# Optimization experiments

Hardware: AMD Instinct MI355X
Metric: run time of the kernel (lower is better)

The kernel has to match this reference:

```python
import jax, jax.numpy as jnp
import numpy as np

BN_EPS = 1e-5

def _square_distance(a, b):
    # a: (B,N,3), b: (B,M,3) -> (B,N,M) squared euclidean distance
    a2 = jnp.sum(a * a, axis=-1)[:, :, None]
    b2 = jnp.sum(b * b, axis=-1)[:, None, :]
    return a2 + b2 - 2.0 * jnp.einsum('bnd,bmd->bnm', a, b)

def _bn(x, gamma, beta, mean, var):
    # eval-mode batchnorm over channel (last) dim
    return (x - mean) * jax.lax.rsqrt(var + BN_EPS) * gamma + beta

def setup_inputs() -> dict:
    key = jax.random.key(0)
    ks = jax.random.split(key, 16)
    B, M, N, D, C = 4, 2048, 16384, 64, 64
    din, dout = C + D, 64
    return {
        'xyz_down': jax.random.normal(ks[0], (B, M, 3), jnp.float32),
        'xyz_up': jax.random.normal(ks[1], (B, N, 3), jnp.float32),
        'feat_down': jax.random.normal(ks[2], (B, M, D), jnp.float32),
        'feat_up': jax.random.normal(ks[3], (B, N, C), jnp.float32),
        'W1': jax.random.normal(ks[4], (din, din), jnp.float32) * 0.05,
        'b1': jax.random.normal(ks[5], (din,), jnp.float32) * 0.05,
        'bn1_gamma': jax.random.uniform(ks[6], (din,), jnp.float32, 0.5, 1.5),
        'bn1_beta': jax.random.normal(ks[7], (din,), jnp.float32) * 0.05,
        'bn1_mean': jax.random.normal(ks[8], (din,), jnp.float32) * 0.05,
        'bn1_var': jax.random.uniform(ks[9], (din,), jnp.float32, 0.5, 1.5),
        'W2': jax.random.normal(ks[10], (dout, din), jnp.float32) * 0.05,
        'b2': jax.random.normal(ks[11], (dout,), jnp.float32) * 0.05,
        'bn2_gamma': jax.random.uniform(ks[12], (dout,), jnp.float32, 0.5, 1.5),
        'bn2_beta': jax.random.normal(ks[13], (dout,), jnp.float32) * 0.05,
        'bn2_mean': jax.random.normal(ks[14], (dout,), jnp.float32) * 0.05,
        'bn2_var': jax.random.uniform(ks[15], (dout,), jnp.float32, 0.5, 1.5),
    }

def reference(xyz_down, xyz_up, feat_down, feat_up,
              W1, b1, bn1_gamma, bn1_beta, bn1_mean, bn1_var,
              W2, b2, bn2_gamma, bn2_beta, bn2_mean, bn2_var):
    dist = _square_distance(xyz_up, xyz_down)              # (B,N,M)
    dist_recip = 1.0 / (dist + 1e-8)
    weight = dist_recip / jnp.sum(dist_recip, axis=2, keepdims=True)
    # bmm-equivalent of the original broadcast-multiply-sum
    feat_interp = jnp.einsum('bnm,bmd->bnd', weight, feat_down)  # (B,N,D)
    x = jnp.concatenate([feat_up, feat_interp], axis=-1)   # (B,N,C+D)
    # Conv1d(k=1) == pointwise linear over channel dim
    x = jnp.einsum('bnc,oc->bno', x, W1) + b1
    x = jax.nn.relu(_bn(x, bn1_gamma, bn1_beta, bn1_mean, bn1_var))
    x = jnp.einsum('bnc,oc->bno', x, W2) + b2
    x = _bn(x, bn2_gamma, bn2_beta, bn2_mean, bn2_var)
    return x
```

## Files before the change

kernel.cpp:

```cpp
#include <hip/hip_runtime.h>

typedef unsigned short u16;
typedef unsigned int   u32;
typedef unsigned long long u64;

typedef __attribute__((ext_vector_type(8))) short bf16x8;
typedef __attribute__((ext_vector_type(4))) float f32x4;
typedef __attribute__((ext_vector_type(2))) float f32x2;

#define BB 4
#define MM 2048
#define NN 16384
#define DD 64

__device__ __forceinline__ u16 f2bf(float f) {
    union { float f; u32 u; } v; v.f = f;
    u32 r = v.u + 0x7fffu + ((v.u >> 16) & 1u);
    return (u16)(r >> 16);
}

__device__ __forceinline__ u32 pack_trunc(float hi, float lo) {
    union { float f; u32 u; } a, b; a.f = hi; b.f = lo;
    return __builtin_amdgcn_perm(a.u, b.u, 0x07060302);
}

__device__ __forceinline__ u32 pack_rne(float hi, float lo) {
    return (u32)f2bf(lo) | ((u32)f2bf(hi) << 16);
}

__device__ __forceinline__ bf16x8 pack8(float4 p, float4 q) {
    bf16x8 v;
    v[0] = (short)f2bf(p.x); v[1] = (short)f2bf(p.y);
    v[2] = (short)f2bf(p.z); v[3] = (short)f2bf(p.w);
    v[4] = (short)f2bf(q.x); v[5] = (short)f2bf(q.y);
    v[6] = (short)f2bf(q.z); v[7] = (short)f2bf(q.w);
    return v;
}

#define OFF_FDT   0ull
#define OFF_XYZP  1048576ull
#define OFF_W1S   1179648ull
#define OFF_W2S   1212416ull
#define OFF_BN    1228800ull
#define WS_NEED   1230336ull

__global__ __launch_bounds__(256)
void prep6_kernel(const float* __restrict__ xyz_down,
                  const float* __restrict__ feat_down,
                  const float* __restrict__ W1, const float* __restrict__ b1,
                  const float* __restrict__ g1, const float* __restrict__ be1,
                  const float* __restrict__ m1, const float* __restrict__ v1,
                  const float* __restrict__ W2, const float* __restrict__ b2,
                  const float* __restrict__ g2, const float* __restrict__ be2,
                  const float* __restrict__ m2, const float* __restrict__ v2,
                  u16* __restrict__ fdT, float4* __restrict__ xyzP,
                  u16* __restrict__ w1s, u16* __restrict__ w2s,
                  float* __restrict__ bnbuf)
{
    const int blk = blockIdx.x, t = threadIdx.x;
    if (blk < 256) {
        __shared__ u16 T[32 * 72];
        const int b = blk >> 6, m0 = (blk & 63) * 32;
        {
            const int row = t >> 3, seg = (t & 7) * 8;
            const float4* src = (const float4*)(feat_down + ((size_t)(b * MM + m0 + row)) * 64 + seg);
            float4 v0 = src[0], v1 = src[1];
            bf16x8 pk = pack8(v0, v1);
            *(bf16x8*)&T[row * 72 + seg] = pk;
        }
        __syncthreads();
        {
            const int d = t & 63, w = t >> 6;
            union { u16 h[8]; uint4 q; } o;
#pragma unroll
            for (int j = 0; j < 8; j++) o.h[j] = T[(w * 8 + j) * 72 + d];
            *(uint4*)&fdT[((size_t)(b * 64 + d)) * MM + m0 + w * 8] = o.q;
        }
    } else if (blk < 272) {
        int g = (blk - 256) * 256 + t;
        int b = g >> 10, p = g & 1023;
        const float* s = xyz_down + ((size_t)b * MM + 2 * p) * 3;
        float x0 = s[0], y0 = s[1], z0 = s[2];
        float x1 = s[3], y1 = s[4], z1 = s[5];
        float w0 = x0 * x0 + y0 * y0 + z0 * z0 + 1e-8f;
        float w1v = x1 * x1 + y1 * y1 + z1 * z1 + 1e-8f;
        xyzP[(size_t)g * 2 + 0] = make_float4(-2.f * x0, -2.f * x1, -2.f * y0, -2.f * y1);
        xyzP[(size_t)g * 2 + 1] = make_float4(-2.f * z0, -2.f * z1, w0, w1v);
    } else if (blk < 280) {
        int slot = (blk - 272) * 256 + t;
        int f = slot >> 6, l = slot & 63;
        int kg = f >> 3, ot = f & 7;
        int o = ot * 16 + (l & 15), c = kg * 32 + (l >> 4) * 8;
        const float4* src = (const float4*)(W1 + (size_t)o * 128 + c);
        bf16x8 v = pack8(src[0], src[1]);
        *(bf16x8*)&w1s[(size_t)slot * 8] = v;
    } else if (blk < 284) {
        int slot = (blk - 280) * 256 + t;
        int f = slot >> 6, l = slot & 63;
        int kg = f >> 2, ot = f & 3;
        int o = ot * 16 + (l & 15), c = kg * 32 + (l >> 4) * 8;
        const float4* src = (const float4*)(W2 + (size_t)o * 128 + c);
        bf16x8 v = pack8(src[0], src[1]);
        *(bf16x8*)&w2s[(size_t)slot * 8] = v;
    } else {
        if (t < 128) {
            float a = g1[t] * rsqrtf(v1[t] + 1e-5f);
            bnbuf[t] = a;
            bnbuf[128 + t] = (b1[t] - m1[t]) * a + be1[t];
        } else if (t < 192) {
            int o = t - 128;
            float a = g2[o] * rsqrtf(v2[o] + 1e-5f);
            bnbuf[256 + o] = a;
            bnbuf[320 + o] = (b2[o] - m2[o]) * a + be2[o];
        }
    }
}

__global__ __launch_bounds__(256, 2)
void fused7_kernel(const float* __restrict__ xyz_up,
                   const u16* __restrict__ fdT,
                   const float4* __restrict__ xyzP,
                   const float* __restrict__ feat_up,
                   const u16* __restrict__ w1s,
                   const u16* __restrict__ w2s,
                   const float* __restrict__ bnbuf,
                   float* __restrict__ out)
{
    __shared__ u16   ftbuf[2][64 * 72];
    __shared__ float xyzb[2][32 * 12];
    __shared__ u16   xh[128 * 136];
    __shared__ float bnl[384];

    const int tid = threadIdx.x;
    const int b  = blockIdx.x >> 7;
    const int n0 = (blockIdx.x & 127) * 128;
    const int wave = tid >> 6;
    const int lane = tid & 63;
    const int q    = lane >> 4;
    const int nl   = lane & 15;

    bnl[tid] = bnbuf[tid];
    if (tid < 128) bnl[256 + tid] = bnbuf[256 + tid];

    {
        const int r = tid >> 1, sg = (tid & 1) * 32;
        const float4* fs = (const float4*)(feat_up + ((size_t)(b * NN + n0 + r)) * 64 + sg);
        float4 f0 = fs[0], f1 = fs[1], f2 = fs[2], f3 = fs[3];
        float4 f4 = fs[4], f5 = fs[5], f6 = fs[6], f7 = fs[7];
        uint4 o0, o1;
        o0.x = pack_rne(f0.y, f0.x); o0.y = pack_rne(f0.w, f0.z);
        o0.z = pack_rne(f1.y, f1.x); o0.w = pack_rne(f1.w, f1.z);
        o1.x = pack_rne(f2.y, f2.x); o1.y = pack_rne(f2.w, f2.z);
        o1.z = pack_rne(f3.y, f3.x); o1.w = pack_rne(f3.w, f3.z);
        uint4* xd = (uint4*)&xh[r * 136 + sg];
        xd[0] = o0; xd[1] = o1;
        uint4 o2, o3;
        o2.x = pack_rne(f4.y, f4.x); o2.y = pack_rne(f4.w, f4.z);
        o2.z = pack_rne(f5.y, f5.x); o2.w = pack_rne(f5.w, f5.z);
        o3.x = pack_rne(f6.y, f6.x); o3.y = pack_rne(f6.w, f6.z);
        o3.z = pack_rne(f7.y, f7.x); o3.w = pack_rne(f7.w, f7.z);
        xd[2] = o2; xd[3] = o3;
    }

    float ax[2], ay[2], az[2];
    f32x2 a22[2];
#pragma unroll
    for (int rt = 0; rt < 2; rt++) {
        const int row = n0 + wave * 32 + rt * 16 + nl;
        const float* xu = xyz_up + ((size_t)(b * NN + row)) * 3;
        ax[rt] = xu[0]; ay[rt] = xu[1]; az[rt] = xu[2];
        float a2 = ax[rt] * ax[rt] + ay[rt] * ay[rt] + az[rt] * az[rt];
        a22[rt] = (f32x2){a2, a2};
    }
    const f32x2 eps2 = (f32x2){1e-8f, 1e-8f};

    f32x4 acc[2][4];
#pragma unroll
    for (int rt = 0; rt < 2; rt++)
#pragma unroll
        for (int i = 0; i < 4; i++) acc[rt][i] = (f32x4){0.f, 0.f, 0.f, 0.f};
    f32x4 accd[2];
    accd[0] = (f32x4){0.f, 0.f, 0.f, 0.f};
    accd[1] = (f32x4){0.f, 0.f, 0.f, 0.f};

    bf16x8 ones;
#pragma unroll
    for (int i = 0; i < 8; i++) ones[i] = (short)0x3F80;

    const int sd = tid >> 2, sms = (tid & 3) * 16;
    const u16* fsrc = fdT + ((size_t)(b * 64 + sd)) * MM + sms;
    const float4* xsrc = xyzP + ((size_t)b * 1024 + (tid >> 1)) * 2 + (tid & 1);
    float* xdst = &xyzb[0][0] + (tid >> 1) * 12 + (tid & 1) * 4;

    {
        u16* fd = &ftbuf[0][sd * 72 + sms];
        *(uint4*)fd       = *(const uint4*)(fsrc);
        *(uint4*)(fd + 8) = *(const uint4*)(fsrc + 8);
        if (tid < 64) *(float4*)xdst = xsrc[0];
    }
    __syncthreads();

    for (int c = 0; c < 32; ++c) {
        const int cur = c & 1, nxt = cur ^ 1;
        const bool have_next = (c + 1) < 32;
        uint4 nf0, nf1; float4 nx;
        if (have_next) {
            const int mc = (c + 1) * 64;
            nf0 = *(const uint4*)(fsrc + mc);
            nf1 = *(const uint4*)(fsrc + mc + 8);
            if (tid < 64) nx = xsrc[(size_t)(c + 1) * 64];
        }

#pragma unroll
        for (int kk = 0; kk < 2; kk++) {
            u32 fr[2][4];
#pragma unroll
            for (int jp = 0; jp < 4; jp++) {
                const int pi = kk * 16 + q * 4 + jp;
                const float* base = &xyzb[cur][pi * 12];
                float4 ld0 = *(const float4*)(base);
                float4 ld1 = *(const float4*)(base + 4);
                f32x2 px = (f32x2){ld0.x, ld0.y};
                f32x2 py = (f32x2){ld0.z, ld0.w};
                f32x2 pz = (f32x2){ld1.x, ld1.y};
                f32x2 pw = (f32x2){ld1.z, ld1.w};
#pragma unroll
                for (int rt = 0; rt < 2; rt++) {
                    f32x2 d = __builtin_elementwise_fma(px, (f32x2){ax[rt], ax[rt]},
                              __builtin_elementwise_fma(py, (f32x2){ay[rt], ay[rt]},
                              __builtin_elementwise_fma(pz, (f32x2){az[rt], az[rt]},
                                                        pw + a22[rt])));
                    d = __builtin_elementwise_max(d, eps2);
                    float r0 = __builtin_amdgcn_rcpf(d.x);
                    float r1 = __builtin_amdgcn_rcpf(d.y);
                    fr[rt][jp] = pack_trunc(r1, r0);
                }
            }
            bf16x8 bb[4];
#pragma unroll
            for (int dt = 0; dt < 4; dt++)
                bb[dt] = *(bf16x8*)&ftbuf[cur][(dt * 16 + nl) * 72 + kk * 32 + q * 8];
#pragma unroll
            for (int rt = 0; rt < 2; rt++) {
                union { u32 u[4]; bf16x8 v; } af;
                af.u[0] = fr[rt][0]; af.u[1] = fr[rt][1];
                af.u[2] = fr[rt][2]; af.u[3] = fr[rt][3];
#pragma unroll
                for (int dt = 0; dt < 4; dt++)
                    acc[rt][dt] = __builtin_amdgcn_mfma_f32_16x16x32_bf16(af.v, bb[dt], acc[rt][dt], 0, 0, 0);
                accd[rt] = __builtin_amdgcn_mfma_f32_16x16x32_bf16(af.v, ones, accd[rt], 0, 0, 0);
            }
        }

        if (have_next) {
            u16* fd = &ftbuf[nxt][sd * 72 + sms];
            *(uint4*)fd       = nf0;
            *(uint4*)(fd + 8) = nf1;
            if (tid < 64) *(float4*)(&xyzb[nxt][0] + (tid >> 1) * 12 + (tid & 1) * 4) = nx;
        }
        __syncthreads();
    }

#pragma unroll
    for (int rt = 0; rt < 2; rt++)
#pragma unroll
    for (int reg = 0; reg < 4; reg++) {
        float inv = 1.0f / accd[rt][reg];
        int rl = wave * 32 + rt * 16 + q * 4 + reg;
#pragma unroll
        for (int dt = 0; dt < 4; dt++)
            xh[rl * 136 + 64 + dt * 16 + nl] = f2bf(acc[rt][dt][reg] * inv);
    }

    f32x4 acc1[2][8];
#pragma unroll
    for (int rt = 0; rt < 2; rt++)
#pragma unroll
        for (int i = 0; i < 8; i++) acc1[rt][i] = (f32x4){0.f, 0.f, 0.f, 0.f};
#pragma unroll
    for (int kg = 0; kg < 4; kg++) {
        bf16x8 afr[2];
#pragma unroll
        for (int rt = 0; rt < 2; rt++)
            afr[rt] = *(bf16x8*)&xh[(wave * 32 + rt * 16 + nl) * 136 + kg * 32 + q * 8];
#pragma unroll
        for (int ot = 0; ot < 8; ot++) {
            bf16x8 bf = *(const bf16x8*)(w1s + ((size_t)(kg * 8 + ot) * 64 + lane) * 8);
            acc1[0][ot] = __builtin_amdgcn_mfma_f32_16x16x32_bf16(afr[0], bf, acc1[0][ot], 0, 0, 0);
            acc1[1][ot] = __builtin_amdgcn_mfma_f32_16x16x32_bf16(afr[1], bf, acc1[1][ot], 0, 0, 0);
        }
    }
#pragma unroll
    for (int ot = 0; ot < 8; ot++) {
        int o = ot * 16 + nl;
        float aa = bnl[o], bc = bnl[128 + o];
#pragma unroll
        for (int rt = 0; rt < 2; rt++)
#pragma unroll
        for (int reg = 0; reg < 4; reg++) {
            float v = fmaxf(fmaf(acc1[rt][ot][reg], aa, bc), 0.f);
            xh[(wave * 32 + rt * 16 + q * 4 + reg) * 136 + o] = f2bf(v);
        }
    }

    f32x4 acc2[2][4];
#pragma unroll
    for (int rt = 0; rt < 2; rt++)
#pragma unroll
        for (int i = 0; i < 4; i++) acc2[rt][i] = (f32x4){0.f, 0.f, 0.f, 0.f};
#pragma unroll
    for (int kg = 0; kg < 4; kg++) {
        bf16x8 afr[2];
#pragma unroll
        for (int rt = 0; rt < 2; rt++)
            afr[rt] = *(bf16x8*)&xh[(wave * 32 + rt * 16 + nl) * 136 + kg * 32 + q * 8];
#pragma unroll
        for (int ot = 0; ot < 4; ot++) {
            bf16x8 bf = *(const bf16x8*)(w2s + ((size_t)(kg * 4 + ot) * 64 + lane) * 8);
            acc2[0][ot] = __builtin_amdgcn_mfma_f32_16x16x32_bf16(afr[0], bf, acc2[0][ot], 0, 0, 0);
            acc2[1][ot] = __builtin_amdgcn_mfma_f32_16x16x32_bf16(afr[1], bf, acc2[1][ot], 0, 0, 0);
        }
    }
    float* of = (float*)xh;
#pragma unroll
    for (int ot = 0; ot < 4; ot++) {
        int o = ot * 16 + nl;
        float aa = bnl[256 + o], bc = bnl[320 + o];
#pragma unroll
        for (int rt = 0; rt < 2; rt++)
#pragma unroll
        for (int reg = 0; reg < 4; reg++)
            of[(wave * 32 + rt * 16 + q * 4 + reg) * 68 + o] = fmaf(acc2[rt][ot][reg], aa, bc);
    }

    {
        const int r = tid >> 1, sg = (tid & 1) * 32;
        const float4* sf = (const float4*)&of[r * 68 + sg];
        float4* dst = (float4*)(out + ((size_t)(b * NN + n0 + r)) * 64 + sg);
#pragma unroll
        for (int i = 0; i < 8; i++) dst[i] = sf[i];
    }
}

#define TN 128
#define BM 64
#define RS 72
#define FS 72

__global__ __launch_bounds__(256, 3)
void interp_kernel(const float* __restrict__ xyz_down,
                   const float* __restrict__ xyz_up,
                   const float* __restrict__ feat_down,
                   u16* __restrict__ interp_out)
{
    __shared__ u16   rbuf[TN * RS];
    __shared__ u16   ftbuf[DD * FS];
    __shared__ float xyzb[BM * 3];
    __shared__ float denp[TN * 2];
    __shared__ float invden[TN];

    const int tid = threadIdx.x;
    const int b  = blockIdx.x >> 7;
    const int n0 = (blockIdx.x & 127) * TN;

    const int nl_r = tid >> 1;
    const int half = tid & 1;
    const float* xu = xyz_up + (size_t)(b * NN + n0 + nl_r) * 3;
    const float ax = xu[0], ay = xu[1], az = xu[2];

    denp[tid] = 0.f;

    const int wave = tid >> 6;
    const int lane = tid & 63;
    const int q    = lane >> 4;
    const int nl   = lane & 15;

    f32x4 acc[2][4];
#pragma unroll
    for (int i = 0; i < 2; i++)
#pragma unroll
        for (int j = 0; j < 4; j++) acc[i][j] = (f32x4){0.f, 0.f, 0.f, 0.f};

    const int sm = (tid & 31) * 2;
    const int sd = (tid >> 5) * 8;

    for (int mc = 0; mc < MM; mc += BM) {
        __syncthreads();
        if (tid < 192) xyzb[tid] = xyz_down[(size_t)(b * MM + mc) * 3 + tid];
        {
            const float4* f0 = (const float4*)(feat_down + (size_t)(b * MM + mc + sm) * DD + sd);
            const float4* f1 = (const float4*)(feat_down + (size_t)(b * MM + mc + sm + 1) * DD + sd);
            float4 a0 = f0[0], a1 = f0[1];
            float4 b0 = f1[0], b1 = f1[1];
            float r0[8] = {a0.x, a0.y, a0.z, a0.w, a1.x, a1.y, a1.z, a1.w};
            float r1[8] = {b0.x, b0.y, b0.z, b0.w, b1.x, b1.y, b1.z, b1.w};
#pragma unroll
            for (int j = 0; j < 8; j++) {
                u32 pk = (u32)f2bf(r0[j]) | ((u32)f2bf(r1[j]) << 16);
                *(u32*)&ftbuf[(sd + j) * FS + sm] = pk;
            }
        }
        __syncthreads();
        {
            float dlc = 0.f;
#pragma unroll
            for (int s = 0; s < 4; s++) {
                bf16x8 v;
#pragma unroll
                for (int j = 0; j < 8; j++) {
                    int m = half * 32 + s * 8 + j;
                    float dx = ax - xyzb[3 * m + 0];
                    float dy = ay - xyzb[3 * m + 1];
                    float dz = az - xyzb[3 * m + 2];
                    float d = fmaf(dx, dx, fmaf(dy, dy, dz * dz)) + 1e-8f;
                    float r = __builtin_amdgcn_rcpf(d);
                    dlc += r;
                    v[j] = (short)f2bf(r);
                }
                *(bf16x8*)&rbuf[nl_r * RS + half * 32 + s * 8] = v;
            }
            denp[nl_r * 2 + half] += dlc;
        }
        __syncthreads();
        {
            const int rowbase = wave * 32;
#pragma unroll
            for (int k0 = 0; k0 < BM; k0 += 32) {
                bf16x8 a0 = *(bf16x8*)&rbuf[(rowbase + nl) * RS + k0 + q * 8];
                bf16x8 a1 = *(bf16x8*)&rbuf[(rowbase + 16 + nl) * RS + k0 + q * 8];
#pragma unroll
                for (int dt = 0; dt < 4; dt++) {
                    bf16x8 bb = *(bf16x8*)&ftbuf[(dt * 16 + nl) * FS + k0 + q * 8];
                    acc[0][dt] = __builtin_amdgcn_mfma_f32_16x16x32_bf16(a0, bb, acc[0][dt], 0, 0, 0);
                    acc[1][dt] = __builtin_amdgcn_mfma_f32_16x16x32_bf16(a1, bb, acc[1][dt], 0, 0, 0);
                }
            }
        }
    }

    __syncthreads();
    if (tid < TN) invden[tid] = 1.0f / (denp[tid * 2] + denp[tid * 2 + 1]);
    __syncthreads();
    {
        const int rowbase = wave * 32;
#pragma unroll
        for (int nt = 0; nt < 2; nt++) {
#pragma unroll
            for (int reg = 0; reg < 4; reg++) {
                int nloc = rowbase + nt * 16 + q * 4 + reg;
                float inv = invden[nloc];
                size_t gbase = (size_t)(b * NN + n0 + nloc) * DD;
#pragma unroll
                for (int dt = 0; dt < 4; dt++)
                    interp_out[gbase + dt * 16 + nl] = f2bf(acc[nt][dt][reg] * inv);
            }
        }
    }
}

#define T2 64

__global__ __launch_bounds__(256, 1)
void mlp_kernel(const float* __restrict__ feat_up,
                const u16*   __restrict__ interp,
                const float* __restrict__ W1, const float* __restrict__ b1,
                const float* __restrict__ g1, const float* __restrict__ be1,
                const float* __restrict__ m1, const float* __restrict__ v1,
                const float* __restrict__ W2, const float* __restrict__ b2,
                const float* __restrict__ g2, const float* __restrict__ be2,
                const float* __restrict__ m2, const float* __restrict__ v2,
                float* __restrict__ out)
{
    __shared__ u16 xb[T2 * 136];
    __shared__ u16 hb[T2 * 136];
    __shared__ u16 w1b[128 * 136];
    __shared__ u16 w2b[64 * 136];
    __shared__ float A1[128], Bc1[128], A2[64], Bc2[64];

    const int tid = threadIdx.x;
    const int b  = blockIdx.x >> 8;
    const int n0 = (blockIdx.x & 255) * T2;
    const int wave = tid >> 6;
    const int lane = tid & 63;
    const int q    = lane >> 4;
    const int nl   = lane & 15;

    if (tid < 128) {
        float a = g1[tid] * rsqrtf(v1[tid] + 1e-5f);
        A1[tid]  = a;
        Bc1[tid] = (b1[tid] - m1[tid]) * a + be1[tid];
    } else if (tid < 192) {
        int o = tid - 128;
        float a = g2[o] * rsqrtf(v2[o] + 1e-5f);
        A2[o]  = a;
        Bc2[o] = (b2[o] - m2[o]) * a + be2[o];
    }
    {
        const float4* src = (const float4*)(W1 + (size_t)(tid >> 1) * 128 + (tid & 1) * 64);
        u16* dst = &w1b[(tid >> 1) * 136 + (tid & 1) * 64];
#pragma unroll
        for (int i = 0; i < 8; i++)
            *(bf16x8*)(dst + 8 * i) = pack8(src[2 * i], src[2 * i + 1]);
    }
    {
        const float4* src = (const float4*)(W2 + (size_t)(tid >> 2) * 128 + (tid & 3) * 32);
        u16* dst = &w2b[(tid >> 2) * 136 + (tid & 3) * 32];
#pragma unroll
        for (int i = 0; i < 4; i++)
            *(bf16x8*)(dst + 8 * i) = pack8(src[2 * i], src[2 * i + 1]);
    }
    if (tid < 128) {
        int n = tid >> 1, hf = tid & 1;
        const float4* src = (const float4*)(feat_up + (size_t)(b * NN + n0 + n) * 64 + hf * 32);
        u16* dst = &xb[n * 136 + hf * 32];
#pragma unroll
        for (int i = 0; i < 4; i++)
            *(bf16x8*)(dst + 8 * i) = pack8(src[2 * i], src[2 * i + 1]);
    } else {
        int t2 = tid - 128;
        int n = t2 >> 1, hf = t2 & 1;
        const uint4* src = (const uint4*)(interp + (size_t)(b * NN + n0 + n) * 64 + hf * 32);
        u16* dst = &xb[n * 136 + 64 + hf * 32];
#pragma unroll
        for (int i = 0; i < 4; i++)
            *(uint4*)(dst + 8 * i) = src[i];
    }
    __syncthreads();

    f32x4 acc1[8];
#pragma unroll
    for (int i = 0; i < 8; i++) acc1[i] = (f32x4){0.f, 0.f, 0.f, 0.f};
#pragma unroll
    for (int k0 = 0; k0 < 128; k0 += 32) {
        bf16x8 a = *(bf16x8*)&xb[(wave * 16 + nl) * 136 + k0 + q * 8];
#pragma unroll
        for (int ot = 0; ot < 8; ot++) {
            bf16x8 bb = *(bf16x8*)&w1b[(ot * 16 + nl) * 136 + k0 + q * 8];
            acc1[ot] = __builtin_amdgcn_mfma_f32_16x16x32_bf16(a, bb, acc1[ot], 0, 0, 0);
        }
    }
#pragma unroll
    for (int ot = 0; ot < 8; ot++) {
        int o = ot * 16 + nl;
        float aa = A1[o], bc = Bc1[o];
#pragma unroll
        for (int reg = 0; reg < 4; reg++) {
            float v = fmaxf(fmaf(acc1[ot][reg], aa, bc), 0.f);
            hb[(wave * 16 + q * 4 + reg) * 136 + o] = f2bf(v);
        }
    }
    __syncthreads();

    f32x4 acc2[4];
#pragma unroll
    for (int i = 0; i < 4; i++) acc2[i] = (f32x4){0.f, 0.f, 0.f, 0.f};
#pragma unroll
    for (int k0 = 0; k0 < 128; k0 += 32) {
        bf16x8 a = *(bf16x8*)&hb[(wave * 16 + nl) * 136 + k0 + q * 8];
#pragma unroll
        for (int ot = 0; ot < 4; ot++) {
            bf16x8 bb = *(bf16x8*)&w2b[(ot * 16 + nl) * 136 + k0 + q * 8];
            acc2[ot] = __builtin_amdgcn_mfma_f32_16x16x32_bf16(a, bb, acc2[ot], 0, 0, 0);
        }
    }
#pragma unroll
    for (int ot = 0; ot < 4; ot++) {
        int o = ot * 16 + nl;
        float aa = A2[o], bc = Bc2[o];
#pragma unroll
        for (int reg = 0; reg < 4; reg++)
            out[(size_t)(b * NN + n0 + wave * 16 + q * 4 + reg) * 64 + o] =
                fmaf(acc2[ot][reg], aa, bc);
    }
}

extern "C" void kernel_launch(void* const* d_in, const int* in_sizes, int n_in,
                              void* d_out, int out_size, void* d_ws, size_t ws_size,
                              hipStream_t stream) {
    const float* xyz_down  = (const float*)d_in[0];
    const float* xyz_up    = (const float*)d_in[1];
    const float* feat_down = (const float*)d_in[2];
    const float* feat_up   = (const float*)d_in[3];
    const float* W1  = (const float*)d_in[4];
    const float* b1  = (const float*)d_in[5];
    const float* g1  = (const float*)d_in[6];
    const float* be1 = (const float*)d_in[7];
    const float* m1  = (const float*)d_in[8];
    const float* v1  = (const float*)d_in[9];
    const float* W2  = (const float*)d_in[10];
    const float* b2  = (const float*)d_in[11];
    const float* g2  = (const float*)d_in[12];
    const float* be2 = (const float*)d_in[13];
    const float* m2  = (const float*)d_in[14];
    const float* v2  = (const float*)d_in[15];
    float* out = (float*)d_out;
    char* ws = (char*)d_ws;

    if (ws_size >= WS_NEED) {
        u16*    fdT   = (u16*)(ws + OFF_FDT);
        float4* xyzP  = (float4*)(ws + OFF_XYZP);
        u16*    w1s   = (u16*)(ws + OFF_W1S);
        u16*    w2s   = (u16*)(ws + OFF_W2S);
        float*  bnbuf = (float*)(ws + OFF_BN);

        prep6_kernel<<<dim3(285), dim3(256), 0, stream>>>(
            xyz_down, feat_down, W1, b1, g1, be1, m1, v1,
            W2, b2, g2, be2, m2, v2, fdT, xyzP, w1s, w2s, bnbuf);
        fused7_kernel<<<dim3(BB * (NN / 128)), dim3(256), 0, stream>>>(
            xyz_up, fdT, xyzP, feat_up, w1s, w2s, bnbuf, out);
    } else {
        u16* interp = (u16*)d_ws;
        interp_kernel<<<dim3(BB * (NN / TN)), dim3(256), 0, stream>>>(
            xyz_down, xyz_up, feat_down, interp);
        mlp_kernel<<<dim3(BB * (NN / T2)), dim3(256), 0, stream>>>(
            feat_up, interp, W1, b1, g1, be1, m1, v1,
            W2, b2, g2, be2, m2, v2, out);
    }
}
```

Baseline: 148.8 us.

## Split interpolation K-dimension across two wave halves with 512-thread blocks

Doubles the block to 512 threads. The two halves of the waves each process half of every 64-point chunk of the M reduction, and their partial accumulators and denominators are combined through shared memory before normalization. Shared buffers are aliased into one smem region to cut LDS use, the feat_up load is deferred until after the main loop, and the MLP stage is split so each wave handles 16 rows. The aim is higher occupancy and more parallelism per tile, at the cost of an extra LDS reduction and more barriers.

```diff
diff --git a/kernel.cpp b/kernel.cpp
--- a/kernel.cpp
+++ b/kernel.cpp
@@ -116,8 +116,8 @@
     }
 }
 
-__global__ __launch_bounds__(256, 2)
-void fused7_kernel(const float* __restrict__ xyz_up,
+__global__ __launch_bounds__(512, 4)
+void fused8_kernel(const float* __restrict__ xyz_up,
                    const u16* __restrict__ fdT,
                    const float4* __restrict__ xyzP,
                    const float* __restrict__ feat_up,
@@ -126,168 +126,179 @@
                    const float* __restrict__ bnbuf,
                    float* __restrict__ out)
 {
-    __shared__ u16   ftbuf[2][64 * 72];
-    __shared__ float xyzb[2][32 * 12];
-    __shared__ u16   xh[128 * 136];
+    __shared__ __align__(16) char smem[34816];
     __shared__ float bnl[384];
-
-    const int tid = threadIdx.x;
-    const int b  = blockIdx.x >> 7;
-    const int n0 = (blockIdx.x & 127) * 128;
+    u16*   const ftbuf = (u16*)smem;
+    float* const xyzb  = (float*)(smem + 18432);
+    u16*   const xh    = (u16*)smem;
+    float* const of    = (float*)smem;
+
+    const int tid  = threadIdx.x;
+    const int b    = blockIdx.x >> 7;
+    const int n0   = (blockIdx.x & 127) * 128;
     const int wave = tid >> 6;
     const int lane = tid & 63;
     const int q    = lane >> 4;
     const int nl   = lane & 15;
-
-    bnl[tid] = bnbuf[tid];
-    if (tid < 128) bnl[256 + tid] = bnbuf[256 + tid];
+    const int rg   = wave & 3;
+    const int h    = wave >> 2;
+
+    if (tid < 384) bnl[tid] = bnbuf[tid];
+
+    float ax[2], ay[2], az[2];
+    f32x2 a22[2];
+#pragma unroll
+    for (int rt = 0; rt < 2; rt++) {
+        const int row = n0 + rg * 32 + rt * 16 + nl;
+        const float* xu = xyz_up + ((size_t)(b * NN + row)) * 3;
+        ax[rt] = xu[0]; ay[rt] = xu[1]; az[rt] = xu[2];
+        float a2 = ax[rt] * ax[rt] + ay[rt] * ay[rt] + az[rt] * az[rt];
+        a22[rt] = (f32x2){a2, a2};
+    }
+    const f32x2 eps2 = (f32x2){1e-8f, 1e-8f};
+
+    f32x4 acc[2][4];
+#pragma unroll
+    for (int rt = 0; rt < 2; rt++)
+#pragma unroll
+        for (int i = 0; i < 4; i++) acc[rt][i] = (f32x4){0.f, 0.f, 0.f, 0.f};
+    f32x4 accd[2];
+    accd[0] = (f32x4){0.f, 0.f, 0.f, 0.f};
+    accd[1] = (f32x4){0.f, 0.f, 0.f, 0.f};
+
+    bf16x8 ones;
+#pragma unroll
+    for (int i = 0; i < 8; i++) ones[i] = (short)0x3F80;
+
+    const int sd = tid >> 3, sms = (tid & 7) * 8;
+    const u16* fsrc = fdT + ((size_t)(b * 64 + sd)) * MM + sms;
+    const float4* xsrc = xyzP + ((size_t)b * 1024 + (tid >> 1)) * 2 + (tid & 1);
 
     {
-        const int r = tid >> 1, sg = (tid & 1) * 32;
-        const float4* fs = (const float4*)(feat_up + ((size_t)(b * NN + n0 + r)) * 64 + sg);
-        float4 f0 = fs[0], f1 = fs[1], f2 = fs[2], f3 = fs[3];
-        float4 f4 = fs[4], f5 = fs[5], f6 = fs[6], f7 = fs[7];
+        *(uint4*)&ftbuf[sd * 72 + sms] = *(const uint4*)fsrc;
+        if (tid < 64)
+            *(float4*)&xyzb[(tid >> 1) * 12 + (tid & 1) * 4] = xsrc[0];
+    }
+    __syncthreads();
+
+    for (int c = 0; c < 32; ++c) {
+        const int cur = c & 1, nxt = cur ^ 1;
+        const bool have_next = (c + 1) < 32;
+        uint4 nf; float4 nx;
+        if (have_next) {
+            nf = *(const uint4*)(fsrc + (c + 1) * 64);
+            if (tid < 64) nx = xsrc[(size_t)(c + 1) * 64];
+        }
+
+        u32 fr[2][4];
+#pragma unroll
+        for (int jp = 0; jp < 4; jp++) {
+            const int pi = h * 16 + q * 4 + jp;
+            const float* base = &xyzb[cur * 384 + pi * 12];
+            float4 ld0 = *(const float4*)(base);
+            float4 ld1 = *(const float4*)(base + 4);
+            f32x2 px = (f32x2){ld0.x, ld0.y};
+            f32x2 py = (f32x2){ld0.z, ld0.w};
+            f32x2 pz = (f32x2){ld1.x, ld1.y};
+            f32x2 pw = (f32x2){ld1.z, ld1.w};
+#pragma unroll
+            for (int rt = 0; rt < 2; rt++) {
+                f32x2 d = __builtin_elementwise_fma(px, (f32x2){ax[rt], ax[rt]},
+                          __builtin_elementwise_fma(py, (f32x2){ay[rt], ay[rt]},
+                          __builtin_elementwise_fma(pz, (f32x2){az[rt], az[rt]},
+                                                    pw + a22[rt])));
+                d = __builtin_elementwise_max(d, eps2);
+                float r0 = __builtin_amdgcn_rcpf(d.x);
+                float r1 = __builtin_amdgcn_rcpf(d.y);
+                fr[rt][jp] = pack_trunc(r1, r0);
+            }
+        }
+        bf16x8 bb[4];
+#pragma unroll
+        for (int dt = 0; dt < 4; dt++)
+            bb[dt] = *(bf16x8*)&ftbuf[cur * 4608 + (dt * 16 + nl) * 72 + h * 32 + q * 8];
+#pragma unroll
+        for (int rt = 0; rt < 2; rt++) {
+            union { u32 u[4]; bf16x8 v; } af;
+            af.u[0] = fr[rt][0]; af.u[1] = fr[rt][1];
+            af.u[2] = fr[rt][2]; af.u[3] = fr[rt][3];
+#pragma unroll
+            for (int dt = 0; dt < 4; dt++)
+                acc[rt][dt] = __builtin_amdgcn_mfma_f32_16x16x32_bf16(af.v, bb[dt], acc[rt][dt], 0, 0, 0);
+            accd[rt] = __builtin_amdgcn_mfma_f32_16x16x32_bf16(af.v, ones, accd[rt], 0, 0, 0);
+        }
+
+        if (have_next) {
+            *(uint4*)&ftbuf[nxt * 4608 + sd * 72 + sms] = nf;
+            if (tid < 64)
+                *(float4*)&xyzb[nxt * 384 + (tid >> 1) * 12 + (tid & 1) * 4] = nx;
+        }
+        __syncthreads();
+    }
+
+    const int fur = tid >> 2, fsg = (tid & 3) * 16;
+    const float4* fup = (const float4*)(feat_up + ((size_t)(b * NN + n0 + fur)) * 64 + fsg);
+    float4 f0 = fup[0], f1 = fup[1], f2 = fup[2], f3 = fup[3];
+
+    if (h) {
+#pragma unroll
+        for (int rt = 0; rt < 2; rt++)
+#pragma unroll
+        for (int reg = 0; reg < 4; reg++) {
+            int row = rg * 32 + rt * 16 + q * 4 + reg;
+#pragma unroll
+            for (int dt = 0; dt < 4; dt++)
+                of[row * 68 + dt * 16 + nl] = acc[rt][dt][reg];
+            if (nl == 0) of[row * 68 + 64] = accd[rt][reg];
+        }
+    }
+    __syncthreads();
+    if (!h) {
+#pragma unroll
+        for (int rt = 0; rt < 2; rt++)
+#pragma unroll
+        for (int reg = 0; reg < 4; reg++) {
+            int row = rg * 32 + rt * 16 + q * 4 + reg;
+#pragma unroll
+            for (int dt = 0; dt < 4; dt++)
+                acc[rt][dt][reg] += of[row * 68 + dt * 16 + nl];
+            accd[rt][reg] += of[row * 68 + 64];
+        }
+    }
+    __syncthreads();
+    if (!h) {
+#pragma unroll
+        for (int rt = 0; rt < 2; rt++)
+#pragma unroll
+        for (int reg = 0; reg < 4; reg++) {
+            float inv = 1.0f / accd[rt][reg];
+            int row = rg * 32 + rt * 16 + q * 4 + reg;
+#pragma unroll
+            for (int dt = 0; dt < 4; dt++)
+                xh[row * 136 + 64 + dt * 16 + nl] = f2bf(acc[rt][dt][reg] * inv);
+        }
+    }
+    {
         uint4 o0, o1;
         o0.x = pack_rne(f0.y, f0.x); o0.y = pack_rne(f0.w, f0.z);
         o0.z = pack_rne(f1.y, f1.x); o0.w = pack_rne(f1.w, f1.z);
         o1.x = pack_rne(f2.y, f2.x); o1.y = pack_rne(f2.w, f2.z);
         o1.z = pack_rne(f3.y, f3.x); o1.w = pack_rne(f3.w, f3.z);
-        uint4* xd = (uint4*)&xh[r * 136 + sg];
+        uint4* xd = (uint4*)&xh[fur * 136 + fsg];
         xd[0] = o0; xd[1] = o1;
-        uint4 o2, o3;
-        o2.x = pack_rne(f4.y, f4.x); o2.y = pack_rne(f4.w, f4.z);
-        o2.z = pack_rne(f5.y, f5.x); o2.w = pack_rne(f5.w, f5.z);
-        o3.x = pack_rne(f6.y, f6.x); o3.y = pack_rne(f6.w, f6.z);
-        o3.z = pack_rne(f7.y, f7.x); o3.w = pack_rne(f7.w, f7.z);
-        xd[2] = o2; xd[3] = o3;
-    }
-
-    float ax[2], ay[2], az[2];
-    f32x2 a22[2];
-#pragma unroll
-    for (int rt = 0; rt < 2; rt++) {
-        const int row = n0 + wave * 32 + rt * 16 + nl;
-        const float* xu = xyz_up + ((size_t)(b * NN + row)) * 3;
-        ax[rt] = xu[0]; ay[rt] = xu[1]; az[rt] = xu[2];
-        float a2 = ax[rt] * ax[rt] + ay[rt] * ay[rt] + az[rt] * az[rt];
-        a22[rt] = (f32x2){a2, a2};
-    }
-    const f32x2 eps2 = (f32x2){1e-8f, 1e-8f};
-
-    f32x4 acc[2][4];
-#pragma unroll
-    for (int rt = 0; rt < 2; rt++)
-#pragma unroll
-        for (int i = 0; i < 4; i++) acc[rt][i] = (f32x4){0.f, 0.f, 0.f, 0.f};
-    f32x4 accd[2];
-    accd[0] = (f32x4){0.f, 0.f, 0.f, 0.f};
-    accd[1] = (f32x4){0.f, 0.f, 0.f, 0.f};
-
-    bf16x8 ones;
-#pragma unroll
-    for (int i = 0; i < 8; i++) ones[i] = (short)0x3F80;
-
-    const int sd = tid >> 2, sms = (tid & 3) * 16;
-    const u16* fsrc = fdT + ((size_t)(b * 64 + sd)) * MM + sms;
-    const float4* xsrc = xyzP + ((size_t)b * 1024 + (tid >> 1)) * 2 + (tid & 1);
-    float* xdst = &xyzb[0][0] + (tid >> 1) * 12 + (tid & 1) * 4;
-
-    {
-        u16* fd = &ftbuf[0][sd * 72 + sms];
-        *(uint4*)fd       = *(const uint4*)(fsrc);
-        *(uint4*)(fd + 8) = *(const uint4*)(fsrc + 8);
-        if (tid < 64) *(float4*)xdst = xsrc[0];
-    }
-    __syncthreads();
-
-    for (int c = 0; c < 32; ++c) {
-        const int cur = c & 1, nxt = cur ^ 1;
-        const bool have_next = (c + 1) < 32;
-        uint4 nf0, nf1; float4 nx;
-        if (have_next) {
-            const int mc = (c + 1) * 64;
-            nf0 = *(const uint4*)(fsrc + mc);
-            nf1 = *(const uint4*)(fsrc + mc + 8);
-            if (tid < 64) nx = xsrc[(size_t)(c + 1) * 64];
-        }
-
-#pragma unroll
-        for (int kk = 0; kk < 2; kk++) {
-            u32 fr[2][4];
-#pragma unroll
-            for (int jp = 0; jp < 4; jp++) {
-                const int pi = kk * 16 + q * 4 + jp;
-                const float* base = &xyzb[cur][pi * 12];
-                float4 ld0 = *(const float4*)(base);
-                float4 ld1 = *(const float4*)(base + 4);
-                f32x2 px = (f32x2){ld0.x, ld0.y};
-                f32x2 py = (f32x2){ld0.z, ld0.w};
-                f32x2 pz = (f32x2){ld1.x, ld1.y};
-                f32x2 pw = (f32x2){ld1.z, ld1.w};
-#pragma unroll
-                for (int rt = 0; rt < 2; rt++) {
-                    f32x2 d = __builtin_elementwise_fma(px, (f32x2){ax[rt], ax[rt]},
-                              __builtin_elementwise_fma(py, (f32x2){ay[rt], ay[rt]},
-                              __builtin_elementwise_fma(pz, (f32x2){az[rt], az[rt]},
-                                                        pw + a22[rt])));
-                    d = __builtin_elementwise_max(d, eps2);
-                    float r0 = __builtin_amdgcn_rcpf(d.x);
-                    float r1 = __builtin_amdgcn_rcpf(d.y);
-                    fr[rt][jp] = pack_trunc(r1, r0);
-                }
-            }
-            bf16x8 bb[4];
-#pragma unroll
-            for (int dt = 0; dt < 4; dt++)
-                bb[dt] = *(bf16x8*)&ftbuf[cur][(dt * 16 + nl) * 72 + kk * 32 + q * 8];
-#pragma unroll
-            for (int rt = 0; rt < 2; rt++) {
-                union { u32 u[4]; bf16x8 v; } af;
-                af.u[0] = fr[rt][0]; af.u[1] = fr[rt][1];
-                af.u[2] = fr[rt][2]; af.u[3] = fr[rt][3];
-#pragma unroll
-                for (int dt = 0; dt < 4; dt++)
-                    acc[rt][dt] = __builtin_amdgcn_mfma_f32_16x16x32_bf16(af.v, bb[dt], acc[rt][dt], 0, 0, 0);
-                accd[rt] = __builtin_amdgcn_mfma_f32_16x16x32_bf16(af.v, ones, accd[rt], 0, 0, 0);
-            }
-        }
-
-        if (have_next) {
-            u16* fd = &ftbuf[nxt][sd * 72 + sms];
-            *(uint4*)fd       = nf0;
-            *(uint4*)(fd + 8) = nf1;
-            if (tid < 64) *(float4*)(&xyzb[nxt][0] + (tid >> 1) * 12 + (tid & 1) * 4) = nx;
-        }
-        __syncthreads();
-    }
-
-#pragma unroll
-    for (int rt = 0; rt < 2; rt++)
-#pragma unroll
-    for (int reg = 0; reg < 4; reg++) {
-        float inv = 1.0f / accd[rt][reg];
-        int rl = wave * 32 + rt * 16 + q * 4 + reg;
-#pragma unroll
-        for (int dt = 0; dt < 4; dt++)
-            xh[rl * 136 + 64 + dt * 16 + nl] = f2bf(acc[rt][dt][reg] * inv);
-    }
-
-    f32x4 acc1[2][8];
-#pragma unroll
-    for (int rt = 0; rt < 2; rt++)
-#pragma unroll
-        for (int i = 0; i < 8; i++) acc1[rt][i] = (f32x4){0.f, 0.f, 0.f, 0.f};
+    }
+    __syncthreads();
+
+    f32x4 acc1[8];
+#pragma unroll
+    for (int i = 0; i < 8; i++) acc1[i] = (f32x4){0.f, 0.f, 0.f, 0.f};
 #pragma unroll
     for (int kg = 0; kg < 4; kg++) {
-        bf16x8 afr[2];
-#pragma unroll
-        for (int rt = 0; rt < 2; rt++)
-            afr[rt] = *(bf16x8*)&xh[(wave * 32 + rt * 16 + nl) * 136 + kg * 32 + q * 8];
+        bf16x8 afr = *(bf16x8*)&xh[(wave * 16 + nl) * 136 + kg * 32 + q * 8];
 #pragma unroll
         for (int ot = 0; ot < 8; ot++) {
             bf16x8 bf = *(const bf16x8*)(w1s + ((size_t)(kg * 8 + ot) * 64 + lane) * 8);
-            acc1[0][ot] = __builtin_amdgcn_mfma_f32_16x16x32_bf16(afr[0], bf, acc1[0][ot], 0, 0, 0);
-            acc1[1][ot] = __builtin_amdgcn_mfma_f32_16x16x32_bf16(afr[1], bf, acc1[1][ot], 0, 0, 0);
+            acc1[ot] = __builtin_amdgcn_mfma_f32_16x16x32_bf16(afr, bf, acc1[ot], 0, 0, 0);
         }
     }
 #pragma unroll
@@ -295,50 +306,38 @@
         int o = ot * 16 + nl;
         float aa = bnl[o], bc = bnl[128 + o];
 #pragma unroll
-        for (int rt = 0; rt < 2; rt++)
-#pragma unroll
         for (int reg = 0; reg < 4; reg++) {
-            float v = fmaxf(fmaf(acc1[rt][ot][reg], aa, bc), 0.f);
-            xh[(wave * 32 + rt * 16 + q * 4 + reg) * 136 + o] = f2bf(v);
-        }
-    }
-
-    f32x4 acc2[2][4];
-#pragma unroll
-    for (int rt = 0; rt < 2; rt++)
-#pragma unroll
-        for (int i = 0; i < 4; i++) acc2[rt][i] = (f32x4){0.f, 0.f, 0.f, 0.f};
+            float v = fmaxf(fmaf(acc1[ot][reg], aa, bc), 0.f);
+            xh[(wave * 16 + q * 4 + reg) * 136 + o] = f2bf(v);
+        }
+    }
+
+    f32x4 acc2[4];
+#pragma unroll
+    for (int i = 0; i < 4; i++) acc2[i] = (f32x4){0.f, 0.f, 0.f, 0.f};
 #pragma unroll
     for (int kg = 0; kg < 4; kg++) {
-        bf16x8 afr[2];
-#pragma unroll
-        for (int rt = 0; rt < 2; rt++)
-            afr[rt] = *(bf16x8*)&xh[(wave * 32 + rt * 16 + nl) * 136 + kg * 32 + q * 8];
+        bf16x8 afr = *(bf16x8*)&xh[(wave * 16 + nl) * 136 + kg * 32 + q * 8];
 #pragma unroll
         for (int ot = 0; ot < 4; ot++) {
             bf16x8 bf = *(const bf16x8*)(w2s + ((size_t)(kg * 4 + ot) * 64 + lane) * 8);
-            acc2[0][ot] = __builtin_amdgcn_mfma_f32_16x16x32_bf16(afr[0], bf, acc2[0][ot], 0, 0, 0);
-            acc2[1][ot] = __builtin_amdgcn_mfma_f32_16x16x32_bf16(afr[1], bf, acc2[1][ot], 0, 0, 0);
-        }
-    }
-    float* of = (float*)xh;
+            acc2[ot] = __builtin_amdgcn_mfma_f32_16x16x32_bf16(afr, bf, acc2[ot], 0, 0, 0);
+        }
+    }
 #pragma unroll
     for (int ot = 0; ot < 4; ot++) {
         int o = ot * 16 + nl;
         float aa = bnl[256 + o], bc = bnl[320 + o];
 #pragma unroll
-        for (int rt = 0; rt < 2; rt++)
-#pragma unroll
         for (int reg = 0; reg < 4; reg++)
-            of[(wave * 32 + rt * 16 + q * 4 + reg) * 68 + o] = fmaf(acc2[rt][ot][reg], aa, bc);
+            of[(wave * 16 + q * 4 + reg) * 68 + o] = fmaf(acc2[ot][reg], aa, bc);
     }
 
     {
-        const int r = tid >> 1, sg = (tid & 1) * 32;
-        const float4* sf = (const float4*)&of[r * 68 + sg];
-        float4* dst = (float4*)(out + ((size_t)(b * NN + n0 + r)) * 64 + sg);
-#pragma unroll
-        for (int i = 0; i < 8; i++) dst[i] = sf[i];
+        const float4* sf = (const float4*)&of[fur * 68 + fsg];
+        float4* dst = (float4*)(out + ((size_t)(b * NN + n0 + fur)) * 64 + fsg);
+#pragma unroll
+        for (int i = 0; i < 4; i++) dst[i] = sf[i];
     }
 }
 
@@ -606,7 +605,7 @@
         prep6_kernel<<<dim3(285), dim3(256), 0, stream>>>(
             xyz_down, feat_down, W1, b1, g1, be1, m1, v1,
             W2, b2, g2, be2, m2, v2, fdT, xyzP, w1s, w2s, bnbuf);
-        fused7_kernel<<<dim3(BB * (NN / 128)), dim3(256), 0, stream>>>(
+        fused8_kernel<<<dim3(BB * (NN / 128)), dim3(512), 0, stream>>>(
             xyz_up, fdT, xyzP, feat_up, w1s, w2s, bnbuf, out);
     } else {
         u16* interp = (u16*)d_ws;
```

Measured after the change: 145.1 us. -2.5%, faster.
